# Kernel optimization log

Measured on AMD Instinct MI355X. Metric: run time of the kernel, lower is better.

Reference implementation:

```python
import jax, jax.numpy as jnp
import numpy as np

N_NODES = 100000
N_EDGES = 1600000
IN_FEAT = 256
OUT_FEAT = 64


def setup_inputs() -> dict:
    key = jax.random.key(0)
    k1, k2, k3, k4, k5 = jax.random.split(key, 5)
    feat = jax.random.normal(k1, (N_NODES, IN_FEAT), dtype=jnp.float32)
    # Xavier-uniform-like init for the weight
    limit = float(np.sqrt(6.0 / (IN_FEAT + OUT_FEAT)))
    weight = jax.random.uniform(k2, (IN_FEAT, OUT_FEAT), dtype=jnp.float32,
                                minval=-limit, maxval=limit)
    # Sparse adjacency in COO form: rows sorted for segment_sum efficiency
    adj_rows = jnp.sort(jax.random.randint(k3, (N_EDGES,), 0, N_NODES, dtype=jnp.int64))
    adj_cols = jax.random.randint(k4, (N_EDGES,), 0, N_NODES, dtype=jnp.int64)
    adj_vals = jax.random.uniform(k5, (N_EDGES,), dtype=jnp.float32)
    return {"feat": feat, "weight": weight, "adj_rows": adj_rows,
            "adj_cols": adj_cols, "adj_vals": adj_vals}


def reference(feat, weight, adj_rows, adj_cols, adj_vals):
    # out = adj @ (feat @ W), adj sparse COO -> gather + weighted scatter-add
    proj = feat @ weight                       # [N, out_feat] dense mm
    msgs = adj_vals[:, None] * proj[adj_cols]  # [E, out_feat] gather
    out = jax.ops.segment_sum(msgs, adj_rows, num_segments=feat.shape[0],
                              indices_are_sorted=True)
    return out
```

## Files before the change

### kernel.cpp

```cpp
#include <hip/hip_runtime.h>
#include <cstdint>

#define IN_FEAT 256
#define OUT_FEAT 64

constexpr int EPW = 64;

typedef __attribute__((ext_vector_type(4))) float f32x4;
typedef __attribute__((ext_vector_type(8))) _Float16 f16x8;

union HF8 { _Float16 h[8]; f16x8 v; };

__global__ __launch_bounds__(256) void gemm_proj_mfma(
    const float* __restrict__ feat, const float* __restrict__ W,
    _Float16* __restrict__ projh, int n_rows)
{
    __shared__ _Float16 sWh[8 * 4 * 64 * 8];

    const int lane = threadIdx.x & 63;
    const int wave = threadIdx.x >> 6;
    const int row0 = blockIdx.x * 64 + wave * 16;
    const int kgrp = lane >> 4;
    int ar = row0 + (lane & 15);
    if (ar >= n_rows) ar = n_rows - 1;

    f32x4 fa[16];
    const float* fp = feat + (size_t)ar * IN_FEAT + kgrp * 8;
    #pragma unroll
    for (int ks = 0; ks < 8; ++ks) {
        fa[2 * ks]     = *reinterpret_cast<const f32x4*>(fp + ks * 32);
        fa[2 * ks + 1] = *reinterpret_cast<const f32x4*>(fp + ks * 32 + 4);
    }

    {
        const int c   = threadIdx.x & 63;
        const int kg0 = threadIdx.x >> 6;
        #pragma unroll
        for (int it = 0; it < 8; ++it) {
            const int kg = it * 4 + kg0;
            HF8 tmp;
            #pragma unroll
            for (int j = 0; j < 8; ++j)
                tmp.h[j] = (_Float16)W[(kg * 8 + j) * OUT_FEAT + c];
            const int ks = kg >> 2;
            const int l  = (kg & 3) * 16 + (c & 15);
            const int ct = c >> 4;
            *reinterpret_cast<f16x8*>(&sWh[((ks * 4 + ct) * 64 + l) * 8]) = tmp.v;
        }
    }
    __syncthreads();
    if (row0 >= n_rows) return;

    f32x4 acc[4];
    #pragma unroll
    for (int ct = 0; ct < 4; ++ct) acc[ct] = f32x4{0.f, 0.f, 0.f, 0.f};

    #pragma unroll
    for (int ks = 0; ks < 8; ++ks) {
        HF8 A;
        #pragma unroll
        for (int h = 0; h < 2; ++h) {
            const f32x4 v = fa[2 * ks + h];
            #pragma unroll
            for (int j = 0; j < 4; ++j)
                A.h[h * 4 + j] = (_Float16)v[j];
        }
        #pragma unroll
        for (int ct = 0; ct < 4; ++ct) {
            HF8 B;
            B.v = *reinterpret_cast<const f16x8*>(
                &sWh[((ks * 4 + ct) * 64 + lane) * 8]);
            acc[ct] = __builtin_amdgcn_mfma_f32_16x16x32_f16(A.v, B.v, acc[ct], 0, 0, 0);
        }
    }

    #pragma unroll
    for (int r = 0; r < 4; ++r) {
        const int row = row0 + kgrp * 4 + r;
        if (row < n_rows) {
            #pragma unroll
            for (int ct = 0; ct < 4; ++ct)
                projh[(size_t)row * OUT_FEAT + ct * 16 + (lane & 15)] =
                    (_Float16)acc[ct][r];
        }
    }
}

__global__ __launch_bounds__(256) void gather_scatter(
    const _Float16* __restrict__ projh, const int* __restrict__ rows,
    const int* __restrict__ cols, const float* __restrict__ vals,
    float* __restrict__ out, int n_edges)
{
    const int lane = threadIdx.x & 63;
    const long wid = (long)((blockIdx.x * 256 + threadIdx.x) >> 6);
    const long e0 = wid * EPW;
    if (e0 >= n_edges) return;

    const long ee = (e0 + lane < n_edges) ? (e0 + lane) : (n_edges - 1);
    const int r_v = rows[ee];
    const int c_v = cols[ee];
    const int v_bits = (e0 + lane < n_edges)
                         ? __builtin_bit_cast(int, vals[ee]) : 0;

    _Float16 p[EPW];
    #pragma unroll
    for (int i = 0; i < EPW; ++i) {
        const int c = __builtin_amdgcn_readlane(c_v, i);
        p[i] = projh[(size_t)c * OUT_FEAT + lane];
    }

    float acc = 0.f;
    int cur = __builtin_amdgcn_readlane(r_v, 0);
    bool first_seg = true;
    #pragma unroll
    for (int i = 0; i < EPW; ++i) {
        const int   r = __builtin_amdgcn_readlane(r_v, i);
        const float v = __builtin_bit_cast(float, __builtin_amdgcn_readlane(v_bits, i));
        if (r != cur) {
            float* dst = out + (size_t)cur * OUT_FEAT + lane;
            if (first_seg) atomicAdd(dst, acc);
            else           *dst = acc;
            first_seg = false;
            acc = 0.f;
            cur = r;
        }
        acc = fmaf(v, (float)p[i], acc);
    }
    atomicAdd(out + (size_t)cur * OUT_FEAT + lane, acc);
}

extern "C" void kernel_launch(void* const* d_in, const int* in_sizes, int n_in,
                              void* d_out, int out_size, void* d_ws, size_t ws_size,
                              hipStream_t stream)
{
    const float* feat     = (const float*)d_in[0];
    const float* weight   = (const float*)d_in[1];
    const int*   adj_rows = (const int*)d_in[2];
    const int*   adj_cols = (const int*)d_in[3];
    const float* adj_vals = (const float*)d_in[4];
    float*       out      = (float*)d_out;
    _Float16*    projh    = (_Float16*)d_ws;

    const int n_nodes = in_sizes[0] / IN_FEAT;
    const int n_edges = in_sizes[2];

    hipMemsetAsync(d_out, 0, (size_t)out_size * sizeof(float), stream);

    const int gemm_blocks = (n_nodes + 63) / 64;
    gemm_proj_mfma<<<gemm_blocks, 256, 0, stream>>>(feat, weight, projh, n_nodes);

    const int waves  = (n_edges + EPW - 1) / EPW;
    const int blocks = (waves + 3) / 4;
    gather_scatter<<<blocks, 256, 0, stream>>>(projh, adj_rows, adj_cols,
                                               adj_vals, out, n_edges);
}
```

Baseline: 65.00 us.

## Persist GEMM grid with tile prefetch, fuse output zeroing, gather 128 edges per wave

```diff
diff --git a/kernel.cpp b/kernel.cpp
--- a/kernel.cpp
+++ b/kernel.cpp
@@ -4,7 +4,7 @@
 #define IN_FEAT 256
 #define OUT_FEAT 64
 
-constexpr int EPW = 64;
+constexpr int GEMM_GRID = 521;
 
 typedef __attribute__((ext_vector_type(4))) float f32x4;
 typedef __attribute__((ext_vector_type(8))) _Float16 f16x8;
@@ -13,24 +13,9 @@
 
 __global__ __launch_bounds__(256) void gemm_proj_mfma(
     const float* __restrict__ feat, const float* __restrict__ W,
-    _Float16* __restrict__ projh, int n_rows)
+    _Float16* __restrict__ projh, float* __restrict__ out, int n_rows)
 {
     __shared__ _Float16 sWh[8 * 4 * 64 * 8];
-
-    const int lane = threadIdx.x & 63;
-    const int wave = threadIdx.x >> 6;
-    const int row0 = blockIdx.x * 64 + wave * 16;
-    const int kgrp = lane >> 4;
-    int ar = row0 + (lane & 15);
-    if (ar >= n_rows) ar = n_rows - 1;
-
-    f32x4 fa[16];
-    const float* fp = feat + (size_t)ar * IN_FEAT + kgrp * 8;
-    #pragma unroll
-    for (int ks = 0; ks < 8; ++ks) {
-        fa[2 * ks]     = *reinterpret_cast<const f32x4*>(fp + ks * 32);
-        fa[2 * ks + 1] = *reinterpret_cast<const f32x4*>(fp + ks * 32 + 4);
-    }
 
     {
         const int c   = threadIdx.x & 63;
@@ -49,40 +34,90 @@
         }
     }
     __syncthreads();
-    if (row0 >= n_rows) return;
-
-    f32x4 acc[4];
-    #pragma unroll
-    for (int ct = 0; ct < 4; ++ct) acc[ct] = f32x4{0.f, 0.f, 0.f, 0.f};
-
-    #pragma unroll
-    for (int ks = 0; ks < 8; ++ks) {
-        HF8 A;
-        #pragma unroll
-        for (int h = 0; h < 2; ++h) {
-            const f32x4 v = fa[2 * ks + h];
-            #pragma unroll
-            for (int j = 0; j < 4; ++j)
-                A.h[h * 4 + j] = (_Float16)v[j];
-        }
-        #pragma unroll
-        for (int ct = 0; ct < 4; ++ct) {
-            HF8 B;
-            B.v = *reinterpret_cast<const f16x8*>(
-                &sWh[((ks * 4 + ct) * 64 + lane) * 8]);
-            acc[ct] = __builtin_amdgcn_mfma_f32_16x16x32_f16(A.v, B.v, acc[ct], 0, 0, 0);
-        }
-    }
-
-    #pragma unroll
-    for (int r = 0; r < 4; ++r) {
-        const int row = row0 + kgrp * 4 + r;
-        if (row < n_rows) {
-            #pragma unroll
-            for (int ct = 0; ct < 4; ++ct)
-                projh[(size_t)row * OUT_FEAT + ct * 16 + (lane & 15)] =
-                    (_Float16)acc[ct][r];
-        }
+
+    const int lane = threadIdx.x & 63;
+    const int wave = threadIdx.x >> 6;
+    const int kgrp = lane >> 4;
+    const int ntiles = (n_rows + 63) >> 6;
+
+    int t = blockIdx.x;
+    if (t >= ntiles) return;
+
+    f32x4 fa[16];
+    {
+        int ar = t * 64 + wave * 16 + (lane & 15);
+        if (ar >= n_rows) ar = n_rows - 1;
+        const float* fp = feat + (size_t)ar * IN_FEAT + kgrp * 8;
+        #pragma unroll
+        for (int ks = 0; ks < 8; ++ks) {
+            fa[2 * ks]     = *reinterpret_cast<const f32x4*>(fp + ks * 32);
+            fa[2 * ks + 1] = *reinterpret_cast<const f32x4*>(fp + ks * 32 + 4);
+        }
+    }
+
+    while (true) {
+        HF8 af[8];
+        #pragma unroll
+        for (int ks = 0; ks < 8; ++ks) {
+            #pragma unroll
+            for (int h = 0; h < 2; ++h) {
+                const f32x4 v = fa[2 * ks + h];
+                #pragma unroll
+                for (int j = 0; j < 4; ++j)
+                    af[ks].h[h * 4 + j] = (_Float16)v[j];
+            }
+        }
+
+        const int tn = t + GEMM_GRID;
+        if (tn < ntiles) {
+            int ar = tn * 64 + wave * 16 + (lane & 15);
+            if (ar >= n_rows) ar = n_rows - 1;
+            const float* fp = feat + (size_t)ar * IN_FEAT + kgrp * 8;
+            #pragma unroll
+            for (int ks = 0; ks < 8; ++ks) {
+                fa[2 * ks]     = *reinterpret_cast<const f32x4*>(fp + ks * 32);
+                fa[2 * ks + 1] = *reinterpret_cast<const f32x4*>(fp + ks * 32 + 4);
+            }
+        }
+
+        f32x4 acc[4];
+        #pragma unroll
+        for (int ct = 0; ct < 4; ++ct) acc[ct] = f32x4{0.f, 0.f, 0.f, 0.f};
+
+        #pragma unroll
+        for (int ks = 0; ks < 8; ++ks) {
+            #pragma unroll
+            for (int ct = 0; ct < 4; ++ct) {
+                HF8 B;
+                B.v = *reinterpret_cast<const f16x8*>(
+                    &sWh[((ks * 4 + ct) * 64 + lane) * 8]);
+                acc[ct] = __builtin_amdgcn_mfma_f32_16x16x32_f16(
+                    af[ks].v, B.v, acc[ct], 0, 0, 0);
+            }
+        }
+
+        const int row0 = t * 64 + wave * 16;
+        #pragma unroll
+        for (int r = 0; r < 4; ++r) {
+            const int row = row0 + kgrp * 4 + r;
+            if (row < n_rows) {
+                #pragma unroll
+                for (int ct = 0; ct < 4; ++ct)
+                    projh[(size_t)row * OUT_FEAT + ct * 16 + (lane & 15)] =
+                        (_Float16)acc[ct][r];
+            }
+        }
+        #pragma unroll
+        for (int i = 0; i < 4; ++i) {
+            const int row = row0 + i * 4 + (lane >> 4);
+            if (row < n_rows)
+                *reinterpret_cast<f32x4*>(
+                    out + (size_t)row0 * OUT_FEAT + i * 256 + lane * 4) =
+                    f32x4{0.f, 0.f, 0.f, 0.f};
+        }
+
+        if (tn >= ntiles) break;
+        t = tn;
     }
 }
 
@@ -93,40 +128,69 @@
 {
     const int lane = threadIdx.x & 63;
     const long wid = (long)((blockIdx.x * 256 + threadIdx.x) >> 6);
-    const long e0 = wid * EPW;
+    const long e0 = wid * 128;
     if (e0 >= n_edges) return;
 
-    const long ee = (e0 + lane < n_edges) ? (e0 + lane) : (n_edges - 1);
-    const int r_v = rows[ee];
-    const int c_v = cols[ee];
-    const int v_bits = (e0 + lane < n_edges)
-                         ? __builtin_bit_cast(int, vals[ee]) : 0;
-
-    _Float16 p[EPW];
+    const long a0 = e0, b0 = e0 + 64;
+    const long eA = (a0 + lane < n_edges) ? (a0 + lane) : (n_edges - 1);
+    const long eB = (b0 + lane < n_edges) ? (b0 + lane) : (n_edges - 1);
+    const int rA = rows[eA], cA = cols[eA];
+    const int rB = rows[eB], cB = cols[eB];
+    const int vA = (a0 + lane < n_edges) ? __builtin_bit_cast(int, vals[eA]) : 0;
+    const int vB = (b0 + lane < n_edges) ? __builtin_bit_cast(int, vals[eB]) : 0;
+
+    _Float16 pA[64], pB[64];
     #pragma unroll
-    for (int i = 0; i < EPW; ++i) {
-        const int c = __builtin_amdgcn_readlane(c_v, i);
-        p[i] = projh[(size_t)c * OUT_FEAT + lane];
-    }
-
-    float acc = 0.f;
-    int cur = __builtin_amdgcn_readlane(r_v, 0);
-    bool first_seg = true;
+    for (int i = 0; i < 64; ++i) {
+        const int c = __builtin_amdgcn_readlane(cA, i);
+        pA[i] = projh[(size_t)c * OUT_FEAT + lane];
+    }
     #pragma unroll
-    for (int i = 0; i < EPW; ++i) {
-        const int   r = __builtin_amdgcn_readlane(r_v, i);
-        const float v = __builtin_bit_cast(float, __builtin_amdgcn_readlane(v_bits, i));
-        if (r != cur) {
-            float* dst = out + (size_t)cur * OUT_FEAT + lane;
-            if (first_seg) atomicAdd(dst, acc);
-            else           *dst = acc;
-            first_seg = false;
-            acc = 0.f;
-            cur = r;
-        }
-        acc = fmaf(v, (float)p[i], acc);
-    }
-    atomicAdd(out + (size_t)cur * OUT_FEAT + lane, acc);
+    for (int i = 0; i < 64; ++i) {
+        const int c = __builtin_amdgcn_readlane(cB, i);
+        pB[i] = projh[(size_t)c * OUT_FEAT + lane];
+    }
+
+    {
+        float acc = 0.f;
+        int cur = __builtin_amdgcn_readlane(rA, 0);
+        bool first_seg = true;
+        #pragma unroll
+        for (int i = 0; i < 64; ++i) {
+            const int   r = __builtin_amdgcn_readlane(rA, i);
+            const float v = __builtin_bit_cast(float, __builtin_amdgcn_readlane(vA, i));
+            if (r != cur) {
+                float* dst = out + (size_t)cur * OUT_FEAT + lane;
+                if (first_seg) atomicAdd(dst, acc);
+                else           *dst = acc;
+                first_seg = false;
+                acc = 0.f;
+                cur = r;
+            }
+            acc = fmaf(v, (float)pA[i], acc);
+        }
+        atomicAdd(out + (size_t)cur * OUT_FEAT + lane, acc);
+    }
+    {
+        float acc = 0.f;
+        int cur = __builtin_amdgcn_readlane(rB, 0);
+        bool first_seg = true;
+        #pragma unroll
+        for (int i = 0; i < 64; ++i) {
+            const int   r = __builtin_amdgcn_readlane(rB, i);
+            const float v = __builtin_bit_cast(float, __builtin_amdgcn_readlane(vB, i));
+            if (r != cur) {
+                float* dst = out + (size_t)cur * OUT_FEAT + lane;
+                if (first_seg) atomicAdd(dst, acc);
+                else           *dst = acc;
+                first_seg = false;
+                acc = 0.f;
+                cur = r;
+            }
+            acc = fmaf(v, (float)pB[i], acc);
+        }
+        atomicAdd(out + (size_t)cur * OUT_FEAT + lane, acc);
+    }
 }
 
 extern "C" void kernel_launch(void* const* d_in, const int* in_sizes, int n_in,
@@ -144,12 +208,12 @@
     const int n_nodes = in_sizes[0] / IN_FEAT;
     const int n_edges = in_sizes[2];
 
-    hipMemsetAsync(d_out, 0, (size_t)out_size * sizeof(float), stream);
-
-    const int gemm_blocks = (n_nodes + 63) / 64;
-    gemm_proj_mfma<<<gemm_blocks, 256, 0, stream>>>(feat, weight, projh, n_nodes);
-
-    const int waves  = (n_edges + EPW - 1) / EPW;
+    const int ntiles = (n_nodes + 63) / 64;
+    const int gemm_blocks = (ntiles < GEMM_GRID) ? ntiles : GEMM_GRID;
+    gemm_proj_mfma<<<gemm_blocks, 256, 0, stream>>>(feat, weight, projh, out,
+                                                    n_nodes);
+
+    const int waves  = (n_edges + 127) / 128;
     const int blocks = (waves + 3) / 4;
     gather_scatter<<<blocks, 256, 0, stream>>>(projh, adj_rows, adj_cols,
                                                adj_vals, out, n_edges);
```

Result: slower. 73.47 us (+13.0%).
